# Kernel tuning notes

Measured on AMD Instinct MI355X. Metric: run time of the kernel, lower is better.

The kernel has to match this reference:

```python
import jax, jax.numpy as jnp
import numpy as np

BIG = 1e10  # sentinel for invalid pairwise distances


def get_xyz(depth, fx, fy, cx, cy):
    # depth: [B,1,H,W] -> xyz: [B,3,H,W] via pinhole unprojection
    B, _, H, W = depth.shape
    v = jnp.arange(H, dtype=depth.dtype)[:, None]   # rows
    u = jnp.arange(W, dtype=depth.dtype)[None, :]   # cols
    z = depth[:, 0]                                  # [B,H,W]
    x = (u - cx) / fx * z
    y = (v - cy) / fy * z
    return jnp.stack([x, y, z], axis=1)              # [B,3,H,W]


def _chamfer_item(p, g, vp, vg):
    # p,g: [N,3] point sets; vp,vg: [N] bool validity masks
    # squared pairwise distances via ||p||^2 + ||g||^2 - 2 p.g
    d = (jnp.sum(p * p, -1)[:, None] + jnp.sum(g * g, -1)[None, :]
         - 2.0 * (p @ g.T))                          # [N,N]
    d = jnp.maximum(d, 0.0)
    has_g = jnp.any(vg)
    has_p = jnp.any(vp)
    d1 = jnp.min(jnp.where(vg[None, :], d, BIG), axis=1)  # per pred point
    d2 = jnp.min(jnp.where(vp[:, None], d, BIG), axis=0)  # per gt point
    s1 = jnp.sum(jnp.where(vp & has_g, d1, 0.0))
    s2 = jnp.sum(jnp.where(vg & has_p, d2, 0.0))
    return s1 + s2


def reference(pred, gt_xyz, mask, fx, fy, cx, cy):
    B = pred.shape[0]
    pred_xyz = get_xyz(pred, fx, fy, cx, cy)             # [B,3,H,W]
    p = pred_xyz.reshape(B, 3, -1).transpose(0, 2, 1)    # [B,N,3]
    g = gt_xyz.reshape(B, 3, -1).transpose(0, 2, 1)      # [B,N,3]
    m = mask[:, 0].reshape(B, -1) > 0                    # [B,N]
    # ignore_zeros=True: drop points whose coordinate sum is exactly 0
    vp = m & (jnp.sum(p, -1) != 0)
    vg = m & (jnp.sum(g, -1) != 0)
    per_item = jax.vmap(_chamfer_item)(p, g, vp, vg)     # [B]
    return jnp.sum(per_item) / B


def setup_inputs() -> dict:
    key = jax.random.key(0)
    k1, k2, k3 = jax.random.split(key, 3)
    B, H, W = 2, 128, 128
    pred = jax.random.uniform(k1, (B, 1, H, W), dtype=jnp.float32) * 2.0 + 0.1
    gt_xyz = jax.random.normal(k2, (B, 3, H, W), dtype=jnp.float32)
    mask = jax.random.randint(k3, (B, 1, H, W), 0, 2, dtype=jnp.int32)
    fx = jnp.float32(525.0)
    fy = jnp.float32(525.0)
    cx = jnp.float32(64.0)
    cy = jnp.float32(64.0)
    return {"pred": pred, "gt_xyz": gt_xyz, "mask": mask,
            "fx": fx, "fy": fy, "cx": cx, "cy": cy}
```

## Files before the change

### kernel.cpp

```cpp
#include <hip/hip_runtime.h>

#define B_ITEMS 2
#define W_IMG   128
#define N_PTS   16384
#define QS      2
#define CH_GRID 2048
#define BIGF    3.4e38f

__global__ __launch_bounds__(256) void prep_kernel(
        const float* __restrict__ pred,
        const float* __restrict__ gt,
        const int*   __restrict__ mask,
        const float* fxp, const float* fyp,
        const float* cxp, const float* cyp,
        int*    __restrict__ cnt,
        float4* __restrict__ pR, float4* __restrict__ gR,
        float4* __restrict__ pT, float4* __restrict__ gT,
        float*  __restrict__ rmG,
        float*  __restrict__ out) {
    int s    = blockIdx.x >> 6;
    int b    = s & 1;
    int isG  = s >> 1;
    int tid  = threadIdx.x;
    int idx  = (blockIdx.x & 63) * 256 + tid;
    int lane = tid & 63, w = tid >> 6;

    if (blockIdx.x == 0 && tid == 0) out[0] = 0.0f;
    rmG[(blockIdx.x << 8) + tid] = BIGF;

    float x, y, z;
    if (!isG) {
        float fx = *fxp, fy = *fyp, cx = *cxp, cy = *cyp;
        float u = (float)(idx & (W_IMG - 1));
        float v = (float)(idx >> 7);
        z = pred[b * N_PTS + idx];
        x = (u - cx) / fx * z;
        y = (v - cy) / fy * z;
    } else {
        x = gt[(b * 3 + 0) * N_PTS + idx];
        y = gt[(b * 3 + 1) * N_PTS + idx];
        z = gt[(b * 3 + 2) * N_PTS + idx];
    }
    int  mv = mask[b * N_PTS + idx];
    bool ok = (mv > 0) && (((x + y) + z) != 0.0f);

    unsigned long long bal = __ballot(ok);
    int nw  = __popcll(bal);
    int pre = __popcll(bal & ((1ull << lane) - 1ull));

    __shared__ int wbase[4];
    __shared__ int blockbase;
    if (lane == 0) wbase[w] = nw;
    __syncthreads();
    if (tid == 0) {
        int s0 = 0;
#pragma unroll
        for (int i = 0; i < 4; ++i) { int t = wbase[i]; wbase[i] = s0; s0 += t; }
        blockbase = s0 ? atomicAdd(&cnt[s], s0) : 0;
    }
    __syncthreads();

    if (ok) {
        int pos = blockbase + wbase[w] + pre;
        float ps = fmaf(z, z, fmaf(y, y, x * x));
        float4* __restrict__ raw = (isG ? gR : pR) + b * N_PTS;
        float4* __restrict__ tf  = (isG ? gT : pT) + b * N_PTS;
        raw[pos] = make_float4(x, y, z, ps);
        tf[pos]  = make_float4(-2.0f * x, -2.0f * y, -2.0f * z, ps);
    }
}

__global__ __launch_bounds__(1024) void pad_kernel(
        const int* __restrict__ cnt,
        float4* __restrict__ pT, float4* __restrict__ gT) {
    int s = blockIdx.x;
    float4* arr = ((s >> 1) ? gT : pT) + (s & 1) * N_PTS;
    int n = cnt[s];
    int pos = n + threadIdx.x;
    if (pos < ((n + 1023) & ~1023))
        arr[pos] = make_float4(0.0f, 0.0f, 0.0f, BIGF);
}

#define VMCNT(n) asm volatile("s_waitcnt vmcnt(" #n ")" ::: "memory")

__device__ __forceinline__ void stage_tile(const float4* __restrict__ src,
                                           float4* lds_base, int w, int lane) {
    const float4* s0 = src + w * 128 + lane;
    __builtin_amdgcn_global_load_lds(
        (const __attribute__((address_space(1))) void*)(s0),
        (__attribute__((address_space(3))) void*)(lds_base + w * 128), 16, 0, 0);
    __builtin_amdgcn_global_load_lds(
        (const __attribute__((address_space(1))) void*)(s0 + 64),
        (__attribute__((address_space(3))) void*)(lds_base + w * 128 + 64), 16, 0, 0);
}

__global__ __launch_bounds__(256, 4) void chamfer_kernel(
        const int*    __restrict__ cnt,
        const float4* __restrict__ pR, const float4* __restrict__ gR,
        const float4* __restrict__ pT, const float4* __restrict__ gT,
        float* __restrict__ rmG) {
    int np0 = cnt[0], np1 = cnt[1], ng0 = cnt[2], ng1 = cnt[3];
    int naArr[4] = {np0, ng0, np1, ng1};
    int nbArr[4] = {ng0, np0, ng1, np1};
    const float4* Arow[4] = {pR, gR, pR + N_PTS, gR + N_PTS};
    const float4* Bcol[4] = {gT, pT, gT + N_PTS, pT + N_PTS};

    int units[4];
    int Utot = 0;
#pragma unroll
    for (int i = 0; i < 4; ++i) {
        units[i] = (naArr[i] > 0 && nbArr[i] > 0) ? (((naArr[i] + 63) >> 6) * QS) : 0;
        Utot += units[i];
    }

    int u = blockIdx.x;
    if (u >= Utot) return;
    int s = 0;
    while (u >= units[s]) { u -= units[s]; ++s; }
    int na = naArr[s], nb = nbArr[s];
    const float4* __restrict__ A  = Arow[s];
    const float4* __restrict__ Bp = Bcol[s];
    int q       = u & (QS - 1);
    int rowbase = (u >> 1) * 64;

    int nbPad  = (nb + 1023) & ~1023;
    int Lq     = nbPad >> 1;
    int cb0    = q * Lq;
    int ntiles = Lq >> 9;

    int tid  = threadIdx.x;
    int lane = tid & 63;
    int w    = tid >> 6;
    int tc   = tid & 31, tr = tid >> 5;

    float px[8], py[8], pz[8], rm[8];
#pragma unroll
    for (int a = 0; a < 8; ++a) {
        float4 v = A[rowbase + a * 8 + tr];
        px[a] = v.x; py[a] = v.y; pz[a] = v.z;
        rm[a] = BIGF;
    }

    __shared__ float4 sB[4][512];
    __shared__ float  smin[64];

    const float4* __restrict__ Bq = Bp + cb0;

    if (0 < ntiles) stage_tile(Bq, sB[0], w, lane);
    if (1 < ntiles) stage_tile(Bq + 512, sB[1], w, lane);
    if (2 < ntiles) stage_tile(Bq + 1024, sB[2], w, lane);

#pragma unroll 1
    for (int t = 0; t < ntiles; ++t) {
        int rem = ntiles - 1 - t;
        if (rem >= 2)      { VMCNT(4); }
        else if (rem == 1) { VMCNT(2); }
        else               { VMCNT(0); }
        __builtin_amdgcn_s_barrier();
        __builtin_amdgcn_sched_barrier(0);
        if (t + 3 < ntiles)
            stage_tile(Bq + (t + 3) * 512, sB[(t + 3) & 3], w, lane);
        const float4* bufc = &sB[t & 3][tc];
#pragma unroll
        for (int cb = 0; cb < 16; cb += 2) {
            float4 c0 = bufc[cb * 32];
            float4 c1 = bufc[cb * 32 + 32];
#pragma unroll
            for (int a = 0; a < 8; ++a) {
                float d0 = fmaf(px[a], c0.x,
                             fmaf(py[a], c0.y, fmaf(pz[a], c0.z, c0.w)));
                float d1 = fmaf(px[a], c1.x,
                             fmaf(py[a], c1.y, fmaf(pz[a], c1.z, c1.w)));
                rm[a] = fminf(fminf(rm[a], d0), d1);
            }
        }
    }

#pragma unroll
    for (int a = 0; a < 8; ++a) {
        float v = rm[a];
        v = fminf(v, __shfl_xor(v, 1, 64));
        v = fminf(v, __shfl_xor(v, 2, 64));
        v = fminf(v, __shfl_xor(v, 4, 64));
        v = fminf(v, __shfl_xor(v, 8, 64));
        v = fminf(v, __shfl_xor(v, 16, 64));
        rm[a] = v;
    }
    if (tc == 0) {
#pragma unroll
        for (int a = 0; a < 8; ++a) smin[a * 8 + tr] = rm[a];
    }
    __syncthreads();
    if (tid < 64) {
        int row = rowbase + tid;
        float v  = smin[tid];
        if (row < na) {
            float ps = A[row].w;
            float vr = fmaxf(v + ps, 0.0f);
            atomicMin((int*)&rmG[(s << 14) + row], __float_as_int(vr));
        }
    }
}

__global__ __launch_bounds__(256) void finish_kernel(
        const int*   __restrict__ cnt,
        const float* __restrict__ rmG,
        float*       __restrict__ out) {
    int gid = blockIdx.x * 256 + threadIdx.x;
    int s   = gid >> 14;
    int row = gid & (N_PTS - 1);
    int np0 = cnt[0], np1 = cnt[1], ng0 = cnt[2], ng1 = cnt[3];
    int naArr[4] = {np0, ng0, np1, ng1};
    int nbArr[4] = {ng0, np0, ng1, np1};
    float v = (row < naArr[s] && nbArr[s] > 0) ? rmG[gid] : 0.0f;
#pragma unroll
    for (int off = 32; off > 0; off >>= 1)
        v += __shfl_down(v, off, 64);
    __shared__ float wsum[4];
    if ((threadIdx.x & 63) == 0) wsum[threadIdx.x >> 6] = v;
    __syncthreads();
    if (threadIdx.x == 0) {
        float t = (wsum[0] + wsum[1]) + (wsum[2] + wsum[3]);
        atomicAdd(out, t * (1.0f / B_ITEMS));
    }
}

extern "C" void kernel_launch(void* const* d_in, const int* in_sizes, int n_in,
                              void* d_out, int out_size, void* d_ws, size_t ws_size,
                              hipStream_t stream) {
    const float* pred = (const float*)d_in[0];
    const float* gt   = (const float*)d_in[1];
    const int*   mask = (const int*)  d_in[2];
    const float* fx   = (const float*)d_in[3];
    const float* fy   = (const float*)d_in[4];
    const float* cx   = (const float*)d_in[5];
    const float* cy   = (const float*)d_in[6];
    float* out = (float*)d_out;

    char* ws = (char*)d_ws;
    size_t SEG = (size_t)B_ITEMS * N_PTS * 16;
    int*    cnt = (int*)ws;
    float4* pR  = (float4*)(ws + 256);
    float4* gR  = (float4*)(ws + 256 + SEG);
    float4* pT  = (float4*)(ws + 256 + 2 * SEG);
    float4* gT  = (float4*)(ws + 256 + 3 * SEG);
    float*  rmG = (float*) (ws + 256 + 4 * SEG);

    hipMemsetAsync(cnt, 0, 16, stream);

    prep_kernel<<<dim3(256), 256, 0, stream>>>(
        pred, gt, mask, fx, fy, cx, cy, cnt, pR, gR, pT, gT, rmG, out);

    pad_kernel<<<dim3(4), 1024, 0, stream>>>(cnt, pT, gT);

    chamfer_kernel<<<dim3(CH_GRID), 256, 0, stream>>>(
        cnt, pR, gR, pT, gT, rmG);

    finish_kernel<<<dim3(256), 256, 0, stream>>>(cnt, rmG, out);
}
```

Baseline: 100.8 us.

## Fold padding and final reduction into last-block epilogues to cut kernel launches

```diff
diff --git a/kernel.cpp b/kernel.cpp
--- a/kernel.cpp
+++ b/kernel.cpp
@@ -14,6 +14,7 @@
         const float* fxp, const float* fyp,
         const float* cxp, const float* cyp,
         int*    __restrict__ cnt,
+        int*    __restrict__ pdone,
         float4* __restrict__ pR, float4* __restrict__ gR,
         float4* __restrict__ pT, float4* __restrict__ gT,
         float*  __restrict__ rmG,
@@ -50,6 +51,7 @@
 
     __shared__ int wbase[4];
     __shared__ int blockbase;
+    __shared__ int plast;
     if (lane == 0) wbase[w] = nw;
     __syncthreads();
     if (tid == 0) {
@@ -68,17 +70,22 @@
         raw[pos] = make_float4(x, y, z, ps);
         tf[pos]  = make_float4(-2.0f * x, -2.0f * y, -2.0f * z, ps);
     }
-}
-
-__global__ __launch_bounds__(1024) void pad_kernel(
-        const int* __restrict__ cnt,
-        float4* __restrict__ pT, float4* __restrict__ gT) {
-    int s = blockIdx.x;
-    float4* arr = ((s >> 1) ? gT : pT) + (s & 1) * N_PTS;
-    int n = cnt[s];
-    int pos = n + threadIdx.x;
-    if (pos < ((n + 1023) & ~1023))
-        arr[pos] = make_float4(0.0f, 0.0f, 0.0f, BIGF);
+
+    __syncthreads();
+    __threadfence();
+    if (tid == 0) plast = (atomicAdd(pdone, 1) == 255) ? 1 : 0;
+    __syncthreads();
+    if (plast) {
+#pragma unroll 1
+        for (int s2 = 0; s2 < 4; ++s2) {
+            float4* arr = ((s2 >> 1) ? gT : pT) + (s2 & 1) * N_PTS;
+            int n = __hip_atomic_load(&cnt[s2], __ATOMIC_RELAXED,
+                                      __HIP_MEMORY_SCOPE_AGENT);
+            int nPad = (n + 1023) & ~1023;
+            for (int k = n + tid; k < nPad; k += 256)
+                arr[k] = make_float4(0.0f, 0.0f, 0.0f, BIGF);
+        }
+    }
 }
 
 #define VMCNT(n) asm volatile("s_waitcnt vmcnt(" #n ")" ::: "memory")
@@ -98,7 +105,9 @@
         const int*    __restrict__ cnt,
         const float4* __restrict__ pR, const float4* __restrict__ gR,
         const float4* __restrict__ pT, const float4* __restrict__ gT,
-        float* __restrict__ rmG) {
+        float* __restrict__ rmG,
+        int*   __restrict__ done,
+        float* __restrict__ out) {
     int np0 = cnt[0], np1 = cnt[1], ng0 = cnt[2], ng1 = cnt[3];
     int naArr[4] = {np0, ng0, np1, ng1};
     int nbArr[4] = {ng0, np0, ng1, np1};
@@ -113,115 +122,125 @@
         Utot += units[i];
     }
 
-    int u = blockIdx.x;
-    if (u >= Utot) return;
-    int s = 0;
-    while (u >= units[s]) { u -= units[s]; ++s; }
-    int na = naArr[s], nb = nbArr[s];
-    const float4* __restrict__ A  = Arow[s];
-    const float4* __restrict__ Bp = Bcol[s];
-    int q       = u & (QS - 1);
-    int rowbase = (u >> 1) * 64;
-
-    int nbPad  = (nb + 1023) & ~1023;
-    int Lq     = nbPad >> 1;
-    int cb0    = q * Lq;
-    int ntiles = Lq >> 9;
-
     int tid  = threadIdx.x;
     int lane = tid & 63;
     int w    = tid >> 6;
-    int tc   = tid & 31, tr = tid >> 5;
-
-    float px[8], py[8], pz[8], rm[8];
-#pragma unroll
-    for (int a = 0; a < 8; ++a) {
-        float4 v = A[rowbase + a * 8 + tr];
-        px[a] = v.x; py[a] = v.y; pz[a] = v.z;
-        rm[a] = BIGF;
-    }
 
     __shared__ float4 sB[4][512];
     __shared__ float  smin[64];
-
-    const float4* __restrict__ Bq = Bp + cb0;
-
-    if (0 < ntiles) stage_tile(Bq, sB[0], w, lane);
-    if (1 < ntiles) stage_tile(Bq + 512, sB[1], w, lane);
-    if (2 < ntiles) stage_tile(Bq + 1024, sB[2], w, lane);
+    __shared__ float  wsum[4];
+    __shared__ int    lastFlag;
+
+    int u = blockIdx.x;
+    if (u < Utot) {
+        int s = 0;
+        while (u >= units[s]) { u -= units[s]; ++s; }
+        int na = naArr[s], nb = nbArr[s];
+        const float4* __restrict__ A  = Arow[s];
+        const float4* __restrict__ Bp = Bcol[s];
+        int q       = u & (QS - 1);
+        int rowbase = (u >> 1) * 64;
+
+        int nbPad  = (nb + 1023) & ~1023;
+        int Lq     = nbPad >> 1;
+        int cb0    = q * Lq;
+        int ntiles = Lq >> 9;
+
+        int tc = tid & 31, tr = tid >> 5;
+
+        float px[8], py[8], pz[8], rm[8];
+#pragma unroll
+        for (int a = 0; a < 8; ++a) {
+            float4 v = A[rowbase + a * 8 + tr];
+            px[a] = v.x; py[a] = v.y; pz[a] = v.z;
+            rm[a] = BIGF;
+        }
+
+        const float4* __restrict__ Bq = Bp + cb0;
+
+        if (0 < ntiles) stage_tile(Bq, sB[0], w, lane);
+        if (1 < ntiles) stage_tile(Bq + 512, sB[1], w, lane);
+        if (2 < ntiles) stage_tile(Bq + 1024, sB[2], w, lane);
 
 #pragma unroll 1
-    for (int t = 0; t < ntiles; ++t) {
-        int rem = ntiles - 1 - t;
-        if (rem >= 2)      { VMCNT(4); }
-        else if (rem == 1) { VMCNT(2); }
-        else               { VMCNT(0); }
-        __builtin_amdgcn_s_barrier();
-        __builtin_amdgcn_sched_barrier(0);
-        if (t + 3 < ntiles)
-            stage_tile(Bq + (t + 3) * 512, sB[(t + 3) & 3], w, lane);
-        const float4* bufc = &sB[t & 3][tc];
-#pragma unroll
-        for (int cb = 0; cb < 16; cb += 2) {
-            float4 c0 = bufc[cb * 32];
-            float4 c1 = bufc[cb * 32 + 32];
-#pragma unroll
-            for (int a = 0; a < 8; ++a) {
-                float d0 = fmaf(px[a], c0.x,
-                             fmaf(py[a], c0.y, fmaf(pz[a], c0.z, c0.w)));
-                float d1 = fmaf(px[a], c1.x,
-                             fmaf(py[a], c1.y, fmaf(pz[a], c1.z, c1.w)));
-                rm[a] = fminf(fminf(rm[a], d0), d1);
+        for (int t = 0; t < ntiles; ++t) {
+            int rem = ntiles - 1 - t;
+            if (rem >= 2)      { VMCNT(4); }
+            else if (rem == 1) { VMCNT(2); }
+            else               { VMCNT(0); }
+            __builtin_amdgcn_s_barrier();
+            __builtin_amdgcn_sched_barrier(0);
+            if (t + 3 < ntiles)
+                stage_tile(Bq + (t + 3) * 512, sB[(t + 3) & 3], w, lane);
+            const float4* bufc = &sB[t & 3][tc];
+#pragma unroll
+            for (int cb = 0; cb < 16; cb += 2) {
+                float4 c0 = bufc[cb * 32];
+                float4 c1 = bufc[cb * 32 + 32];
+#pragma unroll
+                for (int a = 0; a < 8; ++a) {
+                    float d0 = fmaf(px[a], c0.x,
+                                 fmaf(py[a], c0.y, fmaf(pz[a], c0.z, c0.w)));
+                    float d1 = fmaf(px[a], c1.x,
+                                 fmaf(py[a], c1.y, fmaf(pz[a], c1.z, c1.w)));
+                    rm[a] = fminf(fminf(rm[a], d0), d1);
+                }
             }
         }
-    }
-
-#pragma unroll
-    for (int a = 0; a < 8; ++a) {
-        float v = rm[a];
-        v = fminf(v, __shfl_xor(v, 1, 64));
-        v = fminf(v, __shfl_xor(v, 2, 64));
-        v = fminf(v, __shfl_xor(v, 4, 64));
-        v = fminf(v, __shfl_xor(v, 8, 64));
-        v = fminf(v, __shfl_xor(v, 16, 64));
-        rm[a] = v;
-    }
-    if (tc == 0) {
-#pragma unroll
-        for (int a = 0; a < 8; ++a) smin[a * 8 + tr] = rm[a];
-    }
-    __syncthreads();
-    if (tid < 64) {
-        int row = rowbase + tid;
-        float v  = smin[tid];
-        if (row < na) {
-            float ps = A[row].w;
-            float vr = fmaxf(v + ps, 0.0f);
-            atomicMin((int*)&rmG[(s << 14) + row], __float_as_int(vr));
-        }
-    }
-}
-
-__global__ __launch_bounds__(256) void finish_kernel(
-        const int*   __restrict__ cnt,
-        const float* __restrict__ rmG,
-        float*       __restrict__ out) {
-    int gid = blockIdx.x * 256 + threadIdx.x;
-    int s   = gid >> 14;
-    int row = gid & (N_PTS - 1);
-    int np0 = cnt[0], np1 = cnt[1], ng0 = cnt[2], ng1 = cnt[3];
-    int naArr[4] = {np0, ng0, np1, ng1};
-    int nbArr[4] = {ng0, np0, ng1, np1};
-    float v = (row < naArr[s] && nbArr[s] > 0) ? rmG[gid] : 0.0f;
-#pragma unroll
-    for (int off = 32; off > 0; off >>= 1)
-        v += __shfl_down(v, off, 64);
-    __shared__ float wsum[4];
-    if ((threadIdx.x & 63) == 0) wsum[threadIdx.x >> 6] = v;
-    __syncthreads();
-    if (threadIdx.x == 0) {
-        float t = (wsum[0] + wsum[1]) + (wsum[2] + wsum[3]);
-        atomicAdd(out, t * (1.0f / B_ITEMS));
+
+#pragma unroll
+        for (int a = 0; a < 8; ++a) {
+            float v = rm[a];
+            v = fminf(v, __shfl_xor(v, 1, 64));
+            v = fminf(v, __shfl_xor(v, 2, 64));
+            v = fminf(v, __shfl_xor(v, 4, 64));
+            v = fminf(v, __shfl_xor(v, 8, 64));
+            v = fminf(v, __shfl_xor(v, 16, 64));
+            rm[a] = v;
+        }
+        if (tc == 0) {
+#pragma unroll
+            for (int a = 0; a < 8; ++a) smin[a * 8 + tr] = rm[a];
+        }
+        __syncthreads();
+        if (tid < 64) {
+            int row = rowbase + tid;
+            float v  = smin[tid];
+            if (row < na) {
+                float ps = A[row].w;
+                float vr = fmaxf(v + ps, 0.0f);
+                atomicMin((int*)&rmG[(s << 14) + row], __float_as_int(vr));
+            }
+        }
+    }
+
+    __syncthreads();
+    __threadfence();
+    if (tid == 0) {
+        int old = atomicAdd(done, 1);
+        lastFlag = (old == (int)gridDim.x - 1) ? 1 : 0;
+    }
+    __syncthreads();
+
+    if (lastFlag) {
+        int* rmGi = (int*)rmG;
+        float acc = 0.0f;
+#pragma unroll 1
+        for (int s2 = 0; s2 < 4; ++s2) {
+            if (nbArr[s2] <= 0) continue;
+            int na2  = naArr[s2];
+            int base = s2 << 14;
+            for (int k = tid; k < na2; k += 256)
+                acc += __int_as_float(__hip_atomic_load(&rmGi[base + k],
+                        __ATOMIC_RELAXED, __HIP_MEMORY_SCOPE_AGENT));
+        }
+#pragma unroll
+        for (int off = 32; off > 0; off >>= 1)
+            acc += __shfl_down(acc, off, 64);
+        if (lane == 0) wsum[tid >> 6] = acc;
+        __syncthreads();
+        if (tid == 0)
+            out[0] = (wsum[0] + wsum[1] + wsum[2] + wsum[3]) * (1.0f / B_ITEMS);
     }
 }
 
@@ -239,22 +258,20 @@
 
     char* ws = (char*)d_ws;
     size_t SEG = (size_t)B_ITEMS * N_PTS * 16;
-    int*    cnt = (int*)ws;
-    float4* pR  = (float4*)(ws + 256);
-    float4* gR  = (float4*)(ws + 256 + SEG);
-    float4* pT  = (float4*)(ws + 256 + 2 * SEG);
-    float4* gT  = (float4*)(ws + 256 + 3 * SEG);
-    float*  rmG = (float*) (ws + 256 + 4 * SEG);
-
-    hipMemsetAsync(cnt, 0, 16, stream);
+    int*    cnt   = (int*)ws;
+    int*    done  = cnt + 4;
+    int*    pdone = cnt + 5;
+    float4* pR    = (float4*)(ws + 256);
+    float4* gR    = (float4*)(ws + 256 + SEG);
+    float4* pT    = (float4*)(ws + 256 + 2 * SEG);
+    float4* gT    = (float4*)(ws + 256 + 3 * SEG);
+    float*  rmG   = (float*) (ws + 256 + 4 * SEG);
+
+    hipMemsetAsync(cnt, 0, 32, stream);
 
     prep_kernel<<<dim3(256), 256, 0, stream>>>(
-        pred, gt, mask, fx, fy, cx, cy, cnt, pR, gR, pT, gT, rmG, out);
-
-    pad_kernel<<<dim3(4), 1024, 0, stream>>>(cnt, pT, gT);
+        pred, gt, mask, fx, fy, cx, cy, cnt, pdone, pR, gR, pT, gT, rmG, out);
 
     chamfer_kernel<<<dim3(CH_GRID), 256, 0, stream>>>(
-        cnt, pR, gR, pT, gT, rmG);
-
-    finish_kernel<<<dim3(256), 256, 0, stream>>>(cnt, rmG, out);
-}
+        cnt, pR, gR, pT, gT, rmG, done, out);
+}
```

Result: slower. 253.1 us (+151.1%).
